# Kernel tuning notes

Hardware: AMD Instinct MI355X
Metric: run time of the kernel (lower is better)

## Reference

```python
import jax, jax.numpy as jnp
import numpy as np

N, E = 50000, 800000
IN_DIM = 256
OUT_DIM = 256
H = 8
D = OUT_DIM // H  # head_dim = 32
SCALE = D ** -0.5
LN_EPS = 1e-5


def _layernorm(x, g, b):
    mu = jnp.mean(x, axis=-1, keepdims=True)
    var = jnp.mean((x - mu) ** 2, axis=-1, keepdims=True)
    return (x - mu) * jax.lax.rsqrt(var + LN_EPS) * g + b


def setup_inputs() -> dict:
    key = jax.random.key(0)
    ks = jax.random.split(key, 12)
    s = 1.0 / np.sqrt(IN_DIM)
    inp = {
        "x": jax.random.normal(ks[0], (N, IN_DIM), jnp.float32),
        "edge_index": jax.random.randint(ks[1], (2, E), 0, N, jnp.int64),
        "batch": jnp.zeros((N,), jnp.int64),
        # weights stored (in, out) so forward is x @ W
        "Wq": jax.random.uniform(ks[2], (IN_DIM, OUT_DIM), jnp.float32, -s, s),
        "Wk": jax.random.uniform(ks[3], (IN_DIM, OUT_DIM), jnp.float32, -s, s),
        "Wv": jax.random.uniform(ks[4], (IN_DIM, OUT_DIM), jnp.float32, -s, s),
        "Wo_w": jax.random.uniform(ks[5], (OUT_DIM, OUT_DIM), jnp.float32, -s, s),
        "Wo_b": jnp.zeros((OUT_DIM,), jnp.float32),
        "ln1_g": jnp.ones((OUT_DIM,), jnp.float32),
        "ln1_b": jnp.zeros((OUT_DIM,), jnp.float32),
        "ln2_g": jnp.ones((OUT_DIM,), jnp.float32),
        "ln2_b": jnp.zeros((OUT_DIM,), jnp.float32),
        "ffn_w1": jax.random.uniform(ks[6], (OUT_DIM, 2 * OUT_DIM), jnp.float32, -s, s),
        "ffn_b1": jnp.zeros((2 * OUT_DIM,), jnp.float32),
        "ffn_w2": jax.random.uniform(ks[7], (2 * OUT_DIM, OUT_DIM), jnp.float32, -s, s),
        "ffn_b2": jnp.zeros((OUT_DIM,), jnp.float32),
    }
    return inp


def reference(x, edge_index, batch, Wq, Wk, Wv, Wo_w, Wo_b, ln1_g, ln1_b,
              ln2_g, ln2_b, ffn_w1, ffn_b1, ffn_w2, ffn_b2):
    n = x.shape[0]
    residual = x  # in_dim == out_dim -> Identity residual_proj
    Q = (x @ Wq).reshape(n, H, D)
    K = (x @ Wk).reshape(n, H, D)
    V = (x @ Wv).reshape(n, H, D)
    src, dst = edge_index[0], edge_index[1]

    # edge scores (E, H)
    scores = jnp.einsum('ehd,ehd->eh', Q[dst], K[src]) * SCALE
    # segmented max per destination node; init zeros matches torch
    # scatter_reduce amax with include_self=True on a zeros buffer
    attn_max = jnp.zeros((n, H), scores.dtype).at[dst].max(scores)
    w = jnp.exp(scores - attn_max[dst])
    attn_sum = jnp.zeros((n, H), w.dtype).at[dst].add(w)
    w = w / (attn_sum[dst] + 1e-8)

    msg = V[src] * w[:, :, None]                      # (E, H, D)
    out = jnp.zeros((n, H, D), msg.dtype).at[dst].add(msg)
    out = out.reshape(n, OUT_DIM) @ Wo_w + Wo_b

    out = _layernorm(residual + out, ln1_g, ln1_b)
    ffn = jax.nn.gelu(out @ ffn_w1 + ffn_b1, approximate=False) @ ffn_w2 + ffn_b2
    out = _layernorm(out + ffn, ln2_g, ln2_b)
    return out
```

## Files before the change

### kernel.cpp

```cpp
#include <hip/hip_runtime.h>
#include <hip/hip_bf16.h>
#include <math.h>

#define NNODES 50000
#define NEDGES 800000
#define DIM 256
#define HID_DIM 512

typedef short bf16x8 __attribute__((ext_vector_type(8)));
typedef float f32x4 __attribute__((ext_vector_type(4)));

__device__ __forceinline__ float to_f(float v) { return v; }
__device__ __forceinline__ float to_f(__hip_bfloat16 v) { return __bfloat162float(v); }
__device__ __forceinline__ float bf2f(unsigned short u) {
    return __uint_as_float(((unsigned)u) << 16);
}
__device__ __forceinline__ unsigned short f2bf_u16(float v) {
    __hip_bfloat16 h = __float2bfloat16(v);
    return __builtin_bit_cast(unsigned short, h);
}

#define GLD(g, l) __builtin_amdgcn_global_load_lds( \
    (const __attribute__((address_space(1))) unsigned int*)(g), \
    (__attribute__((address_space(3))) unsigned int*)(l), 16, 0, 0)

__global__ __launch_bounds__(256) void gemm_bf16_kernel(
    const __hip_bfloat16* __restrict__ A,
    const __hip_bfloat16* __restrict__ BT,
    const float* __restrict__ bias,
    __hip_bfloat16* __restrict__ C,
    int M, int K, int Nc, int act)
{
    __shared__ __align__(16) short As[128 * 32];
    __shared__ __align__(16) short Bs[128 * 32];

    const int nTilesN = Nc >> 7;
    const int bm = blockIdx.x / nTilesN;
    const int bn = blockIdx.x % nTilesN;
    const int m0 = bm << 7, n0 = bn << 7;
    const int t = threadIdx.x;
    const int wave = t >> 6, lane = t & 63;
    const int quad = lane >> 4, l16 = lane & 15;
    const int wm = (wave & 1) << 6, wn = (wave >> 1) << 6;

    f32x4 acc[4][4] = {};

    const int chunk = wave * 64 + lane;
    const int row = chunk >> 2;
    const int kc = (chunk & 3) << 3;
    int gmA0 = m0 + row;       if (gmA0 >= M) gmA0 = M - 1;
    int gmA1 = m0 + row + 64;  if (gmA1 >= M) gmA1 = M - 1;
    const size_t aoff0 = (size_t)gmA0 * K + kc;
    const size_t aoff1 = (size_t)gmA1 * K + kc;
    const size_t boff0 = (size_t)(n0 + row) * K + kc;
    const size_t boff1 = (size_t)(n0 + row + 64) * K + kc;
    short* ldsA0 = &As[(wave * 64) * 8];
    short* ldsA1 = &As[(256 + wave * 64) * 8];
    short* ldsB0 = &Bs[(wave * 64) * 8];
    short* ldsB1 = &Bs[(256 + wave * 64) * 8];

    for (int k0 = 0; k0 < K; k0 += 32) {
        GLD(A + aoff0 + k0, ldsA0);
        GLD(A + aoff1 + k0, ldsA1);
        GLD(BT + boff0 + k0, ldsB0);
        GLD(BT + boff1 + k0, ldsB1);
        __syncthreads();
        bf16x8 af[4], bfr[4];
        #pragma unroll
        for (int i = 0; i < 4; ++i)
            af[i] = *(const bf16x8*)(&As[(wm + i * 16 + l16) * 32 + quad * 8]);
        #pragma unroll
        for (int j = 0; j < 4; ++j)
            bfr[j] = *(const bf16x8*)(&Bs[(wn + j * 16 + l16) * 32 + quad * 8]);
        #pragma unroll
        for (int i = 0; i < 4; ++i)
            #pragma unroll
            for (int j = 0; j < 4; ++j)
                acc[i][j] = __builtin_amdgcn_mfma_f32_16x16x32_bf16(af[i], bfr[j], acc[i][j], 0, 0, 0);
        __syncthreads();
    }

    #pragma unroll
    for (int i = 0; i < 4; ++i) {
        int rbase = m0 + wm + i * 16 + quad * 4;
        #pragma unroll
        for (int r = 0; r < 4; ++r) {
            int rowg = rbase + r;
            if (rowg >= M) continue;
            #pragma unroll
            for (int j = 0; j < 4; ++j) {
                int col = n0 + wn + j * 16 + l16;
                float v = acc[i][j][r];
                if (bias) v += bias[col];
                if (act) v = 0.5f * v * (1.f + erff(v * 0.70710678118654752f));
                C[(size_t)rowg * Nc + col] = __float2bfloat16(v);
            }
        }
    }
}

__global__ void conv_bf16_kernel(const float* __restrict__ in,
                                 __hip_bfloat16* __restrict__ out, int n4)
{
    int i = blockIdx.x * 256 + threadIdx.x;
    if (i < n4) {
        float4 v = ((const float4*)in)[i];
        __hip_bfloat162 p0, p1;
        p0.x = __float2bfloat16(v.x); p0.y = __float2bfloat16(v.y);
        p1.x = __float2bfloat16(v.z); p1.y = __float2bfloat16(v.w);
        ((__hip_bfloat162*)out)[i * 2]     = p0;
        ((__hip_bfloat162*)out)[i * 2 + 1] = p1;
    }
}

__global__ void prep_w_kernel(const float* __restrict__ Wq, const float* __restrict__ Wk,
                              const float* __restrict__ Wv, const float* __restrict__ Wo,
                              const float* __restrict__ f1, const float* __restrict__ f2,
                              __hip_bfloat16* __restrict__ WqkvT, __hip_bfloat16* __restrict__ WoT,
                              __hip_bfloat16* __restrict__ f1T, __hip_bfloat16* __restrict__ f2T)
{
    int b = blockIdx.x, t = threadIdx.x;
    const float* S; __hip_bfloat16* D; int N, K; int idx;
    if (b < 256)       { S = Wq; D = WqkvT;          K = 256; N = 256; idx = b * 256 + t; }
    else if (b < 512)  { S = Wk; D = WqkvT + 65536;  K = 256; N = 256; idx = (b - 256) * 256 + t; }
    else if (b < 768)  { S = Wv; D = WqkvT + 131072; K = 256; N = 256; idx = (b - 512) * 256 + t; }
    else if (b < 1024) { S = Wo; D = WoT;            K = 256; N = 256; idx = (b - 768) * 256 + t; }
    else if (b < 1536) { S = f1; D = f1T;            K = 256; N = 512; idx = (b - 1024) * 256 + t; }
    else               { S = f2; D = f2T;            K = 512; N = 256; idx = (b - 1536) * 256 + t; }
    int k = idx / N, n = idx % N;
    D[(size_t)n * K + k] = __float2bfloat16(S[idx]);
}

__global__ void hist_kernel(const int* __restrict__ dst, int* __restrict__ counts, int E)
{
    int e = blockIdx.x * blockDim.x + threadIdx.x;
    if (e < E) atomicAdd(&counts[dst[e]], 1);
}

__global__ void scan1_kernel(const int* __restrict__ counts, int* __restrict__ starts,
                             int* __restrict__ bsums, int N)
{
    __shared__ int tmp[256];
    int t = threadIdx.x;
    int i = blockIdx.x * 256 + t;
    int v = (i < N) ? counts[i] : 0;
    tmp[t] = v;
    __syncthreads();
    for (int off = 1; off < 256; off <<= 1) {
        int add = (t >= off) ? tmp[t - off] : 0;
        __syncthreads();
        tmp[t] += add;
        __syncthreads();
    }
    if (i < N) starts[i] = tmp[t] - v;
    if (t == 255) bsums[blockIdx.x] = tmp[255];
}

__global__ void scan2_kernel(const int* __restrict__ bsums, int* __restrict__ bexc, int NB)
{
    __shared__ int tmp[256];
    int t = threadIdx.x;
    int v = (t < NB) ? bsums[t] : 0;
    tmp[t] = v;
    __syncthreads();
    for (int off = 1; off < 256; off <<= 1) {
        int add = (t >= off) ? tmp[t - off] : 0;
        __syncthreads();
        tmp[t] += add;
        __syncthreads();
    }
    bexc[t] = tmp[t] - v;
}

__global__ void scan3_kernel(int* __restrict__ starts, const int* __restrict__ bexc,
                             const int* __restrict__ counts, int* __restrict__ cursor, int N)
{
    int t = threadIdx.x;
    int i = blockIdx.x * 256 + t;
    if (i < N) {
        int val = starts[i] + bexc[blockIdx.x];
        starts[i] = val;
        cursor[i] = val;
        if (i == N - 1) starts[N] = val + counts[i];
    }
}

__global__ void scatter_kernel(const int* __restrict__ src, const int* __restrict__ dst,
                               int* __restrict__ cursor, int* __restrict__ csr_src, int E)
{
    int e = blockIdx.x * blockDim.x + threadIdx.x;
    if (e < E) {
        int d = dst[e];
        int slot = atomicAdd(&cursor[d], 1);
        csr_src[slot] = src[e];
    }
}

__global__ __launch_bounds__(256) void attn_kernel(
    const __hip_bfloat16* __restrict__ QKV,
    const int* __restrict__ starts, const int* __restrict__ csr_src,
    __hip_bfloat16* __restrict__ out)
{
    const int n = blockIdx.x * 4 + (threadIdx.x >> 6);
    const int lane = threadIdx.x & 63;
    const int c = lane << 2;
    const size_t qb = (size_t)n * 768;
    ushort4 qv = *(const ushort4*)(QKV + qb + c);
    const float q0 = bf2f(qv.x), q1 = bf2f(qv.y), q2 = bf2f(qv.z), q3 = bf2f(qv.w);
    const int beg = starts[n], end = starts[n + 1];
    const float SC = 0.17677669529663688f;

    float lA = 0.f, a0 = 0.f, a1 = 0.f, a2 = 0.f, a3 = 0.f;
    float lB = 0.f, b0 = 0.f, b1 = 0.f, b2 = 0.f, b3 = 0.f;
    int e = beg;
    for (; e + 2 <= end; e += 2) {
        int s0 = csr_src[e], s1 = csr_src[e + 1];
        const __hip_bfloat16* p0 = QKV + (size_t)s0 * 768 + 256 + c;
        const __hip_bfloat16* p1 = QKV + (size_t)s1 * 768 + 256 + c;
        ushort4 k0v = *(const ushort4*)p0;
        ushort4 k1v = *(const ushort4*)p1;
        ushort4 v0v = *(const ushort4*)(p0 + 256);
        ushort4 v1v = *(const ushort4*)(p1 + 256);
        float dA = q0 * bf2f(k0v.x) + q1 * bf2f(k0v.y) + q2 * bf2f(k0v.z) + q3 * bf2f(k0v.w);
        float dB = q0 * bf2f(k1v.x) + q1 * bf2f(k1v.y) + q2 * bf2f(k1v.z) + q3 * bf2f(k1v.w);
        dA += __shfl_xor(dA, 1, 8); dA += __shfl_xor(dA, 2, 8); dA += __shfl_xor(dA, 4, 8);
        dB += __shfl_xor(dB, 1, 8); dB += __shfl_xor(dB, 2, 8); dB += __shfl_xor(dB, 4, 8);
        float pA = __expf(dA * SC);
        float pB = __expf(dB * SC);
        lA += pA;
        a0 += pA * bf2f(v0v.x); a1 += pA * bf2f(v0v.y);
        a2 += pA * bf2f(v0v.z); a3 += pA * bf2f(v0v.w);
        lB += pB;
        b0 += pB * bf2f(v1v.x); b1 += pB * bf2f(v1v.y);
        b2 += pB * bf2f(v1v.z); b3 += pB * bf2f(v1v.w);
    }
    if (e < end) {
        int s0 = csr_src[e];
        const __hip_bfloat16* p0 = QKV + (size_t)s0 * 768 + 256 + c;
        ushort4 k0v = *(const ushort4*)p0;
        ushort4 v0v = *(const ushort4*)(p0 + 256);
        float dA = q0 * bf2f(k0v.x) + q1 * bf2f(k0v.y) + q2 * bf2f(k0v.z) + q3 * bf2f(k0v.w);
        dA += __shfl_xor(dA, 1, 8); dA += __shfl_xor(dA, 2, 8); dA += __shfl_xor(dA, 4, 8);
        float pA = __expf(dA * SC);
        lA += pA;
        a0 += pA * bf2f(v0v.x); a1 += pA * bf2f(v0v.y);
        a2 += pA * bf2f(v0v.z); a3 += pA * bf2f(v0v.w);
    }
    float l = lA + lB;
    a0 += b0; a1 += b1; a2 += b2; a3 += b3;
    float inv = 1.f / (l + 1e-8f);
    ushort4 o;
    o.x = f2bf_u16(a0 * inv);
    o.y = f2bf_u16(a1 * inv);
    o.z = f2bf_u16(a2 * inv);
    o.w = f2bf_u16(a3 * inv);
    *(ushort4*)(out + (size_t)n * DIM + c) = o;
}

template <typename TA, typename TB>
__global__ __launch_bounds__(256) void ln_kernel(
    const TA* __restrict__ a, const TB* __restrict__ b,
    const float* __restrict__ g, const float* __restrict__ beta,
    float* __restrict__ outf, __hip_bfloat16* __restrict__ outh)
{
    const int n = blockIdx.x;
    const int t = threadIdx.x;
    float x = to_f(a[(size_t)n * DIM + t]) + to_f(b[(size_t)n * DIM + t]);
    float s = x, s2 = x * x;
    #pragma unroll
    for (int off = 32; off >= 1; off >>= 1) {
        s  += __shfl_xor(s,  off, 64);
        s2 += __shfl_xor(s2, off, 64);
    }
    __shared__ float sb[4], sb2[4];
    int w = t >> 6;
    if ((t & 63) == 0) { sb[w] = s; sb2[w] = s2; }
    __syncthreads();
    float tot  = sb[0] + sb[1] + sb[2] + sb[3];
    float tot2 = sb2[0] + sb2[1] + sb2[2] + sb2[3];
    float mean = tot * (1.f / DIM);
    float var  = tot2 * (1.f / DIM) - mean * mean;
    float inv  = rsqrtf(var + 1e-5f);
    float o = (x - mean) * inv * g[t] + beta[t];
    if (outf) outf[(size_t)n * DIM + t] = o;
    if (outh) outh[(size_t)n * DIM + t] = __float2bfloat16(o);
}

extern "C" void kernel_launch(void* const* d_in, const int* in_sizes, int n_in,
                              void* d_out, int out_size, void* d_ws, size_t ws_size,
                              hipStream_t stream)
{
    const float* x     = (const float*)d_in[0];
    const int*   edge  = (const int*)d_in[1];
    const float* Wq    = (const float*)d_in[3];
    const float* Wk    = (const float*)d_in[4];
    const float* Wv    = (const float*)d_in[5];
    const float* Wo_w  = (const float*)d_in[6];
    const float* Wo_b  = (const float*)d_in[7];
    const float* ln1_g = (const float*)d_in[8];
    const float* ln1_b = (const float*)d_in[9];
    const float* ln2_g = (const float*)d_in[10];
    const float* ln2_b = (const float*)d_in[11];
    const float* fw1   = (const float*)d_in[12];
    const float* fb1   = (const float*)d_in[13];
    const float* fw2   = (const float*)d_in[14];
    const float* fb2   = (const float*)d_in[15];
    const int* srcA = edge;
    const int* dstA = edge + NEDGES;

    char* p = (char*)d_ws;
    const size_t QKV_SZ = (size_t)NNODES * 768 * 2;
    const size_t H_SZ   = (size_t)NNODES * DIM * 2;
    const size_t HID_SZ = (size_t)NNODES * HID_DIM * 2;
    __hip_bfloat16* QKVh = (__hip_bfloat16*)p;  p += QKV_SZ;
    __hip_bfloat16* AOh  = (__hip_bfloat16*)p;  p += H_SZ;
    __hip_bfloat16* O1h  = (__hip_bfloat16*)p;  p += H_SZ;
    __hip_bfloat16* HIDh = (__hip_bfloat16*)p;  p += HID_SZ;
    __hip_bfloat16* xh   = (__hip_bfloat16*)p;  p += H_SZ;
    __hip_bfloat16* WOh  = QKVh;
    __hip_bfloat16* FFh  = QKVh + (size_t)NNODES * DIM;
    __hip_bfloat16* WqkvT = (__hip_bfloat16*)p; p += (size_t)768 * 256 * 2;
    __hip_bfloat16* WoT   = (__hip_bfloat16*)p; p += (size_t)256 * 256 * 2;
    __hip_bfloat16* fw1T  = (__hip_bfloat16*)p; p += (size_t)512 * 256 * 2;
    __hip_bfloat16* fw2T  = (__hip_bfloat16*)p; p += (size_t)256 * 512 * 2;
    int* counts = (int*)p;  p += sizeof(int) * NNODES;
    int* starts = (int*)p;  p += sizeof(int) * (NNODES + 1);
    int* bsums  = (int*)p;  p += sizeof(int) * 256;
    int* bexc   = (int*)p;  p += sizeof(int) * 256;
    int* cursor = (int*)p;  p += sizeof(int) * NNODES;
    int* csr    = (int*)p;  p += sizeof(int) * NEDGES;

    const int NB = (NNODES + 255) / 256;
    const int mT = (NNODES + 127) / 128;
    dim3 blk(256);

    conv_bf16_kernel<<<(NNODES * DIM / 4 + 255) / 256, blk, 0, stream>>>(x, xh, NNODES * DIM / 4);
    prep_w_kernel<<<2048, blk, 0, stream>>>(Wq, Wk, Wv, Wo_w, fw1, fw2, WqkvT, WoT, fw1T, fw2T);

    hipMemsetAsync(counts, 0, sizeof(int) * NNODES, stream);
    hist_kernel<<<(NEDGES + 255) / 256, blk, 0, stream>>>(dstA, counts, NEDGES);
    scan1_kernel<<<NB, blk, 0, stream>>>(counts, starts, bsums, NNODES);
    scan2_kernel<<<1, blk, 0, stream>>>(bsums, bexc, NB);
    scan3_kernel<<<NB, blk, 0, stream>>>(starts, bexc, counts, cursor, NNODES);
    scatter_kernel<<<(NEDGES + 255) / 256, blk, 0, stream>>>(srcA, dstA, cursor, csr, NEDGES);

    gemm_bf16_kernel<<<mT * 6, blk, 0, stream>>>(xh, WqkvT, nullptr, QKVh, NNODES, 256, 768, 0);

    attn_kernel<<<NNODES / 4, blk, 0, stream>>>(QKVh, starts, csr, AOh);

    gemm_bf16_kernel<<<mT * 2, blk, 0, stream>>>(AOh, WoT, Wo_b, WOh, NNODES, 256, 256, 0);
    ln_kernel<float, __hip_bfloat16><<<NNODES, blk, 0, stream>>>(x, WOh, ln1_g, ln1_b, nullptr, O1h);

    gemm_bf16_kernel<<<mT * 4, blk, 0, stream>>>(O1h, fw1T, fb1, HIDh, NNODES, 256, 512, 1);
    gemm_bf16_kernel<<<mT * 2, blk, 0, stream>>>(HIDh, fw2T, fb2, FFh, NNODES, 512, 256, 0);
    ln_kernel<__hip_bfloat16, __hip_bfloat16><<<NNODES, blk, 0, stream>>>(O1h, FFh, ln2_g, ln2_b, (float*)d_out, nullptr);
}
```

Measured before the change: 605.1 us.

## Widen GEMM K-tile with swizzled LDS, unroll attention by four, vectorize layernorm

The GEMM now loads a 64-wide K slice per iteration into an XOR-swizzled LDS layout, which halves the number of barriers and is meant to avoid LDS bank conflicts on fragment reads. The attention kernel processes four edges per iteration with separate accumulators, raising memory-level parallelism for the gathered K/V rows. The layernorm kernel now handles one row per wave with 4-wide vector loads and stores and a wave-only reduction, which removes shared memory and the block barrier. The costs are more LDS per block, higher register pressure in the attention loop, and 50000/4 = 12500 LN blocks with no bounds guard, which is still exact here.

```diff
diff --git a/kernel.cpp b/kernel.cpp
--- a/kernel.cpp
+++ b/kernel.cpp
@@ -31,8 +31,8 @@
     __hip_bfloat16* __restrict__ C,
     int M, int K, int Nc, int act)
 {
-    __shared__ __align__(16) short As[128 * 32];
-    __shared__ __align__(16) short Bs[128 * 32];
+    __shared__ __align__(16) short As[128 * 64];
+    __shared__ __align__(16) short Bs[128 * 64];
 
     const int nTilesN = Nc >> 7;
     const int bm = blockIdx.x / nTilesN;
@@ -45,38 +45,46 @@
 
     f32x4 acc[4][4] = {};
 
-    const int chunk = wave * 64 + lane;
-    const int row = chunk >> 2;
-    const int kc = (chunk & 3) << 3;
-    int gmA0 = m0 + row;       if (gmA0 >= M) gmA0 = M - 1;
-    int gmA1 = m0 + row + 64;  if (gmA1 >= M) gmA1 = M - 1;
-    const size_t aoff0 = (size_t)gmA0 * K + kc;
-    const size_t aoff1 = (size_t)gmA1 * K + kc;
-    const size_t boff0 = (size_t)(n0 + row) * K + kc;
-    const size_t boff1 = (size_t)(n0 + row + 64) * K + kc;
-    short* ldsA0 = &As[(wave * 64) * 8];
-    short* ldsA1 = &As[(256 + wave * 64) * 8];
-    short* ldsB0 = &Bs[(wave * 64) * 8];
-    short* ldsB1 = &Bs[(256 + wave * 64) * 8];
-
-    for (int k0 = 0; k0 < K; k0 += 32) {
-        GLD(A + aoff0 + k0, ldsA0);
-        GLD(A + aoff1 + k0, ldsA1);
-        GLD(BT + boff0 + k0, ldsB0);
-        GLD(BT + boff1 + k0, ldsB1);
-        __syncthreads();
-        bf16x8 af[4], bfr[4];
+    const int rr = lane >> 3;
+    const int ch = lane & 7;
+    const int gcol = ((ch ^ rr) << 3);
+    size_t aoff[4], boff[4];
+    #pragma unroll
+    for (int g = 0; g < 4; ++g) {
+        int r = (wave * 4 + g) * 8 + rr;
+        int gm = m0 + r; if (gm >= M) gm = M - 1;
+        aoff[g] = (size_t)gm * K + gcol;
+        boff[g] = (size_t)(n0 + r) * K + gcol;
+    }
+
+    for (int k0 = 0; k0 < K; k0 += 64) {
         #pragma unroll
-        for (int i = 0; i < 4; ++i)
-            af[i] = *(const bf16x8*)(&As[(wm + i * 16 + l16) * 32 + quad * 8]);
+        for (int g = 0; g < 4; ++g)
+            GLD(A + aoff[g] + k0, &As[(wave * 4 + g) * 512]);
         #pragma unroll
-        for (int j = 0; j < 4; ++j)
-            bfr[j] = *(const bf16x8*)(&Bs[(wn + j * 16 + l16) * 32 + quad * 8]);
+        for (int g = 0; g < 4; ++g)
+            GLD(BT + boff[g] + k0, &Bs[(wave * 4 + g) * 512]);
+        __syncthreads();
         #pragma unroll
-        for (int i = 0; i < 4; ++i)
+        for (int kk = 0; kk < 2; ++kk) {
+            bf16x8 af[4], bfv[4];
+            const int cswz = quad + kk * 4;
             #pragma unroll
-            for (int j = 0; j < 4; ++j)
-                acc[i][j] = __builtin_amdgcn_mfma_f32_16x16x32_bf16(af[i], bfr[j], acc[i][j], 0, 0, 0);
+            for (int i = 0; i < 4; ++i) {
+                int row = wm + i * 16 + l16;
+                af[i] = *(const bf16x8*)(&As[row * 64 + ((cswz ^ (row & 7)) << 3)]);
+            }
+            #pragma unroll
+            for (int j = 0; j < 4; ++j) {
+                int row = wn + j * 16 + l16;
+                bfv[j] = *(const bf16x8*)(&Bs[row * 64 + ((cswz ^ (row & 7)) << 3)]);
+            }
+            #pragma unroll
+            for (int i = 0; i < 4; ++i)
+                #pragma unroll
+                for (int j = 0; j < 4; ++j)
+                    acc[i][j] = __builtin_amdgcn_mfma_f32_16x16x32_bf16(af[i], bfv[j], acc[i][j], 0, 0, 0);
+        }
         __syncthreads();
     }
 
@@ -210,31 +218,40 @@
     const int beg = starts[n], end = starts[n + 1];
     const float SC = 0.17677669529663688f;
 
-    float lA = 0.f, a0 = 0.f, a1 = 0.f, a2 = 0.f, a3 = 0.f;
-    float lB = 0.f, b0 = 0.f, b1 = 0.f, b2 = 0.f, b3 = 0.f;
+    float lA = 0.f, lB = 0.f, lC = 0.f, lD = 0.f;
+    f32x4 aA = {0,0,0,0}, aB = {0,0,0,0}, aC = {0,0,0,0}, aD = {0,0,0,0};
     int e = beg;
-    for (; e + 2 <= end; e += 2) {
-        int s0 = csr_src[e], s1 = csr_src[e + 1];
+    for (; e + 4 <= end; e += 4) {
+        int s0 = csr_src[e], s1 = csr_src[e + 1], s2 = csr_src[e + 2], s3 = csr_src[e + 3];
         const __hip_bfloat16* p0 = QKV + (size_t)s0 * 768 + 256 + c;
         const __hip_bfloat16* p1 = QKV + (size_t)s1 * 768 + 256 + c;
+        const __hip_bfloat16* p2 = QKV + (size_t)s2 * 768 + 256 + c;
+        const __hip_bfloat16* p3 = QKV + (size_t)s3 * 768 + 256 + c;
         ushort4 k0v = *(const ushort4*)p0;
         ushort4 k1v = *(const ushort4*)p1;
+        ushort4 k2v = *(const ushort4*)p2;
+        ushort4 k3v = *(const ushort4*)p3;
         ushort4 v0v = *(const ushort4*)(p0 + 256);
         ushort4 v1v = *(const ushort4*)(p1 + 256);
+        ushort4 v2v = *(const ushort4*)(p2 + 256);
+        ushort4 v3v = *(const ushort4*)(p3 + 256);
         float dA = q0 * bf2f(k0v.x) + q1 * bf2f(k0v.y) + q2 * bf2f(k0v.z) + q3 * bf2f(k0v.w);
         float dB = q0 * bf2f(k1v.x) + q1 * bf2f(k1v.y) + q2 * bf2f(k1v.z) + q3 * bf2f(k1v.w);
+        float dC = q0 * bf2f(k2v.x) + q1 * bf2f(k2v.y) + q2 * bf2f(k2v.z) + q3 * bf2f(k2v.w);
+        float dD = q0 * bf2f(k3v.x) + q1 * bf2f(k3v.y) + q2 * bf2f(k3v.z) + q3 * bf2f(k3v.w);
         dA += __shfl_xor(dA, 1, 8); dA += __shfl_xor(dA, 2, 8); dA += __shfl_xor(dA, 4, 8);
         dB += __shfl_xor(dB, 1, 8); dB += __shfl_xor(dB, 2, 8); dB += __shfl_xor(dB, 4, 8);
-        float pA = __expf(dA * SC);
-        float pB = __expf(dB * SC);
-        lA += pA;
-        a0 += pA * bf2f(v0v.x); a1 += pA * bf2f(v0v.y);
-        a2 += pA * bf2f(v0v.z); a3 += pA * bf2f(v0v.w);
-        lB += pB;
-        b0 += pB * bf2f(v1v.x); b1 += pB * bf2f(v1v.y);
-        b2 += pB * bf2f(v1v.z); b3 += pB * bf2f(v1v.w);
-    }
-    if (e < end) {
+        dC += __shfl_xor(dC, 1, 8); dC += __shfl_xor(dC, 2, 8); dC += __shfl_xor(dC, 4, 8);
+        dD += __shfl_xor(dD, 1, 8); dD += __shfl_xor(dD, 2, 8); dD += __shfl_xor(dD, 4, 8);
+        float pA = __expf(dA * SC), pB = __expf(dB * SC);
+        float pC = __expf(dC * SC), pD = __expf(dD * SC);
+        lA += pA; lB += pB; lC += pC; lD += pD;
+        aA[0] += pA * bf2f(v0v.x); aA[1] += pA * bf2f(v0v.y); aA[2] += pA * bf2f(v0v.z); aA[3] += pA * bf2f(v0v.w);
+        aB[0] += pB * bf2f(v1v.x); aB[1] += pB * bf2f(v1v.y); aB[2] += pB * bf2f(v1v.z); aB[3] += pB * bf2f(v1v.w);
+        aC[0] += pC * bf2f(v2v.x); aC[1] += pC * bf2f(v2v.y); aC[2] += pC * bf2f(v2v.z); aC[3] += pC * bf2f(v2v.w);
+        aD[0] += pD * bf2f(v3v.x); aD[1] += pD * bf2f(v3v.y); aD[2] += pD * bf2f(v3v.z); aD[3] += pD * bf2f(v3v.w);
+    }
+    for (; e < end; ++e) {
         int s0 = csr_src[e];
         const __hip_bfloat16* p0 = QKV + (size_t)s0 * 768 + 256 + c;
         ushort4 k0v = *(const ushort4*)p0;
@@ -243,47 +260,65 @@
         dA += __shfl_xor(dA, 1, 8); dA += __shfl_xor(dA, 2, 8); dA += __shfl_xor(dA, 4, 8);
         float pA = __expf(dA * SC);
         lA += pA;
-        a0 += pA * bf2f(v0v.x); a1 += pA * bf2f(v0v.y);
-        a2 += pA * bf2f(v0v.z); a3 += pA * bf2f(v0v.w);
-    }
-    float l = lA + lB;
-    a0 += b0; a1 += b1; a2 += b2; a3 += b3;
+        aA[0] += pA * bf2f(v0v.x); aA[1] += pA * bf2f(v0v.y);
+        aA[2] += pA * bf2f(v0v.z); aA[3] += pA * bf2f(v0v.w);
+    }
+    float l = (lA + lB) + (lC + lD);
+    float o0 = (aA[0] + aB[0]) + (aC[0] + aD[0]);
+    float o1 = (aA[1] + aB[1]) + (aC[1] + aD[1]);
+    float o2 = (aA[2] + aB[2]) + (aC[2] + aD[2]);
+    float o3 = (aA[3] + aB[3]) + (aC[3] + aD[3]);
     float inv = 1.f / (l + 1e-8f);
     ushort4 o;
-    o.x = f2bf_u16(a0 * inv);
-    o.y = f2bf_u16(a1 * inv);
-    o.z = f2bf_u16(a2 * inv);
-    o.w = f2bf_u16(a3 * inv);
+    o.x = f2bf_u16(o0 * inv);
+    o.y = f2bf_u16(o1 * inv);
+    o.z = f2bf_u16(o2 * inv);
+    o.w = f2bf_u16(o3 * inv);
     *(ushort4*)(out + (size_t)n * DIM + c) = o;
 }
 
-template <typename TA, typename TB>
+template <typename TA>
 __global__ __launch_bounds__(256) void ln_kernel(
-    const TA* __restrict__ a, const TB* __restrict__ b,
+    const TA* __restrict__ a, const __hip_bfloat16* __restrict__ b,
     const float* __restrict__ g, const float* __restrict__ beta,
     float* __restrict__ outf, __hip_bfloat16* __restrict__ outh)
 {
-    const int n = blockIdx.x;
-    const int t = threadIdx.x;
-    float x = to_f(a[(size_t)n * DIM + t]) + to_f(b[(size_t)n * DIM + t]);
-    float s = x, s2 = x * x;
+    const int n = blockIdx.x * 4 + (threadIdx.x >> 6);
+    const int lane = threadIdx.x & 63;
+    const int c = lane << 2;
+    float xv[4];
+    ushort4 bv = *(const ushort4*)(b + (size_t)n * DIM + c);
+    xv[0] = bf2f(bv.x); xv[1] = bf2f(bv.y); xv[2] = bf2f(bv.z); xv[3] = bf2f(bv.w);
+    if constexpr (sizeof(TA) == 4) {
+        float4 av = *(const float4*)(a + (size_t)n * DIM + c);
+        xv[0] += av.x; xv[1] += av.y; xv[2] += av.z; xv[3] += av.w;
+    } else {
+        ushort4 av = *(const ushort4*)((const unsigned short*)a + (size_t)n * DIM + c);
+        xv[0] += bf2f(av.x); xv[1] += bf2f(av.y); xv[2] += bf2f(av.z); xv[3] += bf2f(av.w);
+    }
+    float s  = (xv[0] + xv[1]) + (xv[2] + xv[3]);
+    float s2 = (xv[0]*xv[0] + xv[1]*xv[1]) + (xv[2]*xv[2] + xv[3]*xv[3]);
     #pragma unroll
-    for (int off = 32; off >= 1; off >>= 1) {
+    for (int off = 1; off < 64; off <<= 1) {
         s  += __shfl_xor(s,  off, 64);
         s2 += __shfl_xor(s2, off, 64);
     }
-    __shared__ float sb[4], sb2[4];
-    int w = t >> 6;
-    if ((t & 63) == 0) { sb[w] = s; sb2[w] = s2; }
-    __syncthreads();
-    float tot  = sb[0] + sb[1] + sb[2] + sb[3];
-    float tot2 = sb2[0] + sb2[1] + sb2[2] + sb2[3];
-    float mean = tot * (1.f / DIM);
-    float var  = tot2 * (1.f / DIM) - mean * mean;
+    float mean = s * (1.f / DIM);
+    float var  = s2 * (1.f / DIM) - mean * mean;
     float inv  = rsqrtf(var + 1e-5f);
-    float o = (x - mean) * inv * g[t] + beta[t];
-    if (outf) outf[(size_t)n * DIM + t] = o;
-    if (outh) outh[(size_t)n * DIM + t] = __float2bfloat16(o);
+    float4 gv = *(const float4*)(g + c);
+    float4 bt = *(const float4*)(beta + c);
+    float o0 = (xv[0] - mean) * inv * gv.x + bt.x;
+    float o1 = (xv[1] - mean) * inv * gv.y + bt.y;
+    float o2 = (xv[2] - mean) * inv * gv.z + bt.z;
+    float o3 = (xv[3] - mean) * inv * gv.w + bt.w;
+    if (outf) {
+        *(float4*)(outf + (size_t)n * DIM + c) = make_float4(o0, o1, o2, o3);
+    } else {
+        ushort4 o;
+        o.x = f2bf_u16(o0); o.y = f2bf_u16(o1); o.z = f2bf_u16(o2); o.w = f2bf_u16(o3);
+        *(ushort4*)(outh + (size_t)n * DIM + c) = o;
+    }
 }
 
 extern "C" void kernel_launch(void* const* d_in, const int* in_sizes, int n_in,
@@ -349,9 +384,9 @@
     attn_kernel<<<NNODES / 4, blk, 0, stream>>>(QKVh, starts, csr, AOh);
 
     gemm_bf16_kernel<<<mT * 2, blk, 0, stream>>>(AOh, WoT, Wo_b, WOh, NNODES, 256, 256, 0);
-    ln_kernel<float, __hip_bfloat16><<<NNODES, blk, 0, stream>>>(x, WOh, ln1_g, ln1_b, nullptr, O1h);
+    ln_kernel<float><<<(NNODES + 3) / 4, blk, 0, stream>>>(x, WOh, ln1_g, ln1_b, nullptr, O1h);
 
     gemm_bf16_kernel<<<mT * 4, blk, 0, stream>>>(O1h, fw1T, fb1, HIDh, NNODES, 256, 512, 1);
     gemm_bf16_kernel<<<mT * 2, blk, 0, stream>>>(HIDh, fw2T, fb2, FFh, NNODES, 512, 256, 0);
-    ln_kernel<__hip_bfloat16, __hip_bfloat16><<<NNODES, blk, 0, stream>>>(O1h, FFh, ln2_g, ln2_b, (float*)d_out, nullptr);
-}
+    ln_kernel<__hip_bfloat16><<<(NNODES + 3) / 4, blk, 0, stream>>>(O1h, FFh, ln2_g, ln2_b, (float*)d_out, nullptr);
+}
```

Measured after the change: 583.4 us. 3.6% less time.
